# Optimization experiments

Measured on AMD Instinct MI355X. Metric: run time of the kernel, lower is better.

The kernel has to match this reference:

```python
import jax, jax.numpy as jnp
import numpy as np

N = 50000      # nodes
E = 400000     # edges (before self loops)
G = 8          # graphs in the batch
H = 128        # latent width (message_passer out_channels)
F_IN = 5       # raw node features
F_MASK = 3     # mask features (last col = BC indicator)
F_EDGE = 3     # edge_feature_dim
OUT = 3        # x-vel, y-vel, pressure
REPEATS = 3    # message passing rounds


def _mlp2(x, W1, b1, W2, b2):
    return jax.nn.relu(x @ W1 + b1) @ W2 + b2


def _seg_mean(v, ids, num):
    s = jax.ops.segment_sum(v, ids, num_segments=num)
    c = jax.ops.segment_sum(jnp.ones((v.shape[0],), v.dtype), ids, num_segments=num)
    return s / jnp.maximum(c, 1.0)[:, None]


def setup_inputs() -> dict:
    key = jax.random.key(0)
    ks = jax.random.split(key, 16)
    x = jax.random.normal(ks[0], (N, F_IN), jnp.float32)
    x_mask = (jax.random.uniform(ks[1], (N, F_MASK)) < 0.2).astype(jnp.float32)
    edge_index = jax.random.randint(ks[2], (2, E), 0, N, dtype=jnp.int32)
    edge_attr = jax.random.normal(ks[3], (E, F_EDGE), jnp.float32)
    pos = jax.random.uniform(ks[4], (N, 2), dtype=jnp.float32)
    batch = jnp.sort(jax.random.randint(ks[5], (N,), 0, G, dtype=jnp.int32))
    lin = lambda k, i, o: jax.random.normal(k, (i, o), jnp.float32) * (1.0 / np.sqrt(i))
    return {
        'x': x, 'x_mask': x_mask, 'edge_attr': edge_attr, 'pos': pos,
        'W_e1': lin(ks[6], F_IN + F_MASK, H), 'b_e1': jnp.zeros((H,), jnp.float32),
        'W_e2': lin(ks[7], H, H), 'b_e2': jnp.zeros((H,), jnp.float32),
        'W_m1': lin(ks[8], 2 * H + F_EDGE, H), 'b_m1': jnp.zeros((H,), jnp.float32),
        'W_m2': lin(ks[9], H, H), 'b_m2': jnp.zeros((H,), jnp.float32),
        'W_u1': lin(ks[10], 4 * H, H), 'b_u1': jnp.zeros((H,), jnp.float32),
        'W_u2': lin(ks[11], H, H), 'b_u2': jnp.zeros((H,), jnp.float32),
        'W_d1': lin(ks[12], H, H), 'b_d1': jnp.zeros((H,), jnp.float32),
        'W_d2': lin(ks[13], H, OUT), 'b_d2': jnp.zeros((OUT,), jnp.float32),
        'edge_index': edge_index, 'batch': batch,
    }


def reference(x, x_mask, edge_attr, pos,
              W_e1, b_e1, W_e2, b_e2,
              W_m1, b_m1, W_m2, b_m2,
              W_u1, b_u1, W_u2, b_u2,
              W_d1, b_d1, W_d2, b_d2,
              edge_index, batch):
    n = x.shape[0]
    bc = x_mask[:, -1]                                   # BC indicator (0/1)
    h = jnp.concatenate([x, x_mask], axis=1)             # [N, F_IN+F_MASK]
    # add self loops with zero edge attributes
    sl = jnp.arange(n, dtype=edge_index.dtype)
    ei = jnp.concatenate([edge_index, jnp.stack([sl, sl])], axis=1)
    ea = jnp.concatenate([edge_attr, jnp.zeros((n, edge_attr.shape[1]), edge_attr.dtype)], axis=0)
    # encoder
    h = _mlp2(h, W_e1, b_e1, W_e2, b_e2)                 # [N, H]
    # BC scatter-mean per graph and global mean pool
    bc_cnt = jax.ops.segment_sum(bc, batch, num_segments=G)
    x_BC = jax.ops.segment_sum(h * bc[:, None], batch, num_segments=G) / jnp.maximum(bc_cnt, 1.0)[:, None]
    x_graph = _seg_mean(h, batch, G)
    src, dst = ei[0], ei[1]
    for _ in range(REPEATS):
        m = _mlp2(jnp.concatenate([h[src], h[dst], ea], axis=1), W_m1, b_m1, W_m2, b_m2)
        agg = _seg_mean(m, dst, n)                       # mean aggregation at dst
        upd_in = jnp.concatenate([h, agg, x_graph[batch], x_BC[batch]], axis=1)
        h = h + _mlp2(upd_in, W_u1, b_u1, W_u2, b_u2)
        x_graph = _seg_mean(h, batch, G)
    return _mlp2(h, W_d1, b_d1, W_d2, b_d2)              # [N, OUT]
```

## Files before the change

### kernel.cpp

```cpp
#include <hip/hip_runtime.h>


#define NN 50000
#define EE 400000
#define GG 8
#define NBLK 196
#define SGRID 512

typedef __attribute__((ext_vector_type(8))) short short8;
typedef __attribute__((ext_vector_type(4))) float floatx4;

__device__ __forceinline__ unsigned short f2bf(float x) {
    unsigned u = __float_as_uint(x);
    u += 0x7FFF + ((u >> 16) & 1);
    return (unsigned short)(u >> 16);
}
__device__ __forceinline__ float bf2f(unsigned short h) {
    return __uint_as_float(((unsigned)h) << 16);
}
__device__ __forceinline__ void cvt8(const float* v, short8& hi, short8& lo) {
#pragma unroll
    for (int j = 0; j < 8; ++j) {
        unsigned short h = f2bf(v[j]);
        hi[j] = (short)h;
        lo[j] = (short)f2bf(v[j] - bf2f(h));
    }
}

__global__ void k_count(const int* __restrict__ ei, int* __restrict__ deg) {
    int i = blockIdx.x * 256 + threadIdx.x;
    if (i < EE) atomicAdd(&deg[ei[EE + i]], 1);
}

__global__ __launch_bounds__(256) void k_scan1(const int* __restrict__ deg, int* __restrict__ ex,
                                               int* __restrict__ blksum) {
    __shared__ int s[256];
    const int t = threadIdx.x;
    int i = blockIdx.x * 256 + t;
    int v = (i < NN) ? deg[i] : 0;
    s[t] = v;
    __syncthreads();
    for (int off = 1; off < 256; off <<= 1) {
        int x = (t >= off) ? s[t - off] : 0;
        __syncthreads();
        s[t] += x;
        __syncthreads();
    }
    if (i < NN) ex[i] = s[t] - v;
    if (t == 255) blksum[blockIdx.x] = s[255];
}

__global__ __launch_bounds__(256) void k_scan2(int* __restrict__ blksum) {
    __shared__ int s[256];
    const int t = threadIdx.x;
    int v = (t < NBLK) ? blksum[t] : 0;
    s[t] = v;
    __syncthreads();
    for (int off = 1; off < 256; off <<= 1) {
        int x = (t >= off) ? s[t - off] : 0;
        __syncthreads();
        s[t] += x;
        __syncthreads();
    }
    if (t < NBLK) blksum[t] = s[t] - v;
}

__global__ void k_scan3(const int* __restrict__ ex, const int* __restrict__ blkoff,
                        int* __restrict__ row_ptr, int* __restrict__ cursor) {
    int i = blockIdx.x * 256 + threadIdx.x;
    if (i < NN) {
        int v = ex[i] + blkoff[blockIdx.x];
        row_ptr[i] = v;
        cursor[i] = v;
    }
    if (i == 0) row_ptr[NN] = EE;
}

__global__ void k_scatter(const int* __restrict__ ei, const float* __restrict__ ea,
                          int* __restrict__ cursor, int* __restrict__ src_sorted,
                          float4* __restrict__ ea_s) {
    int e = blockIdx.x * 256 + threadIdx.x;
    if (e >= EE) return;
    int s = ei[e], d = ei[EE + e];
    int p = atomicAdd(&cursor[d], 1);
    src_sorted[p] = s;
    ea_s[p] = make_float4(ea[3 * e], ea[3 * e + 1], ea[3 * e + 2], 0.f);
}

__global__ __launch_bounds__(256) void k_counts(const int* __restrict__ batch, const float* __restrict__ xm,
                                                float* __restrict__ cnt_node, float* __restrict__ cnt_bc) {
    __shared__ float cn[8], cb[8];
    const int t = threadIdx.x;
    if (t < 8) { cn[t] = 0.f; cb[t] = 0.f; }
    __syncthreads();
    int i = blockIdx.x * 256 + t;
    if (i < NN) {
        int g = batch[i];
        atomicAdd(&cn[g], 1.f);
        atomicAdd(&cb[g], xm[3 * i + 2]);
    }
    __syncthreads();
    if (t < 8) {
        if (cn[t] != 0.f) atomicAdd(&cnt_node[t], cn[t]);
        if (cb[t] != 0.f) atomicAdd(&cnt_bc[t], cb[t]);
    }
}

__global__ __launch_bounds__(256) void k_wfuse(const float* __restrict__ Wm2, const float* __restrict__ Wu1,
                                               float* __restrict__ Wf) {
    int idx = blockIdx.x * 256 + threadIdx.x;
    int r = idx >> 7, c = idx & 127;
    float s = 0.f;
    for (int k = 0; k < 128; ++k) s += Wm2[r * 128 + k] * Wu1[(128 + k) * 128 + c];
    Wf[idx] = s;
}
__global__ void k_bfuse(const float* __restrict__ bm2, const float* __restrict__ Wu1,
                        const float* __restrict__ bu1, float* __restrict__ bf) {
    int c = threadIdx.x;
    float s = bu1[c];
    for (int k = 0; k < 128; ++k) s += bm2[k] * Wu1[(128 + k) * 128 + c];
    bf[c] = s;
}

__global__ __launch_bounds__(256) void k_pack_all(
    const float* __restrict__ We2, const float* __restrict__ Wm1,
    const float* __restrict__ Wu1, const float* __restrict__ Wf,
    const float* __restrict__ Wu2, const float* __restrict__ Wd1,
    short* __restrict__ We2h, short* __restrict__ We2l,
    short* __restrict__ Wm1sh, short* __restrict__ Wm1sl,
    short* __restrict__ Wm1dh, short* __restrict__ Wm1dl,
    short* __restrict__ Wu1ah, short* __restrict__ Wu1al,
    short* __restrict__ Wfh, short* __restrict__ Wfl,
    short* __restrict__ Wu2h, short* __restrict__ Wu2l,
    short* __restrict__ Wd1h, short* __restrict__ Wd1l) {
    int b = blockIdx.x;
    int id = b >> 6;
    int p = (b & 63) * 256 + threadIdx.x;
    const float* W;
    short *hi, *lo;
    switch (id) {
        case 0: W = We2; hi = We2h; lo = We2l; break;
        case 1: W = Wm1; hi = Wm1sh; lo = Wm1sl; break;
        case 2: W = Wm1 + 16384; hi = Wm1dh; lo = Wm1dl; break;
        case 3: W = Wu1; hi = Wu1ah; lo = Wu1al; break;
        case 4: W = Wf; hi = Wfh; lo = Wfl; break;
        case 5: W = Wu2; hi = Wu2h; lo = Wu2l; break;
        default: W = Wd1; hi = Wd1h; lo = Wd1l; break;
    }
    int j = p & 7;
    int lane = (p >> 3) & 63;
    int chunk = p >> 9;
    int k0 = chunk & 3, nt = chunk >> 2;
    int quad = lane >> 4;
    int n = nt * 16 + (lane & 15);
    int k;
    if (id == 5) k = k0 * 32 + ((j >> 2) << 4) + (quad << 2) + (j & 3);
    else k = k0 * 32 + quad * 8 + j;
    float w = W[k * 128 + n];
    unsigned short h = f2bf(w);
    hi[p] = (short)h;
    lo[p] = (short)f2bf(w - bf2f(h));
}

__global__ __launch_bounds__(256, 2) void k_genc(
    const float* __restrict__ x, const float* __restrict__ xm,
    const float* __restrict__ We1, const float* __restrict__ be1,
    const short* __restrict__ W2h, const short* __restrict__ W2l,
    const float* __restrict__ be2, const int* __restrict__ batch,
    float* __restrict__ hout, float* __restrict__ part_h, float* __restrict__ part_hbc) {
    __shared__ __align__(16) short sWh[16384];
    __shared__ __align__(16) short sWl[16384];
    __shared__ __align__(16) float swe[1024];
    __shared__ float sbe[128];
    __shared__ float ldsH[1024];
    __shared__ float ldsB[1024];
    const int tid = threadIdx.x;
    const int wave = tid >> 6, lane = tid & 63;
    const int m16 = lane & 15, quad = lane >> 4;
    const int t0 = blockIdx.x * 4 + wave;
    const int t1 = t0 + SGRID * 4;
    const bool h1 = (t1 < 3125);
    const int r0 = t0 * 16 + m16;
    const int r1 = (h1 ? t1 * 16 : 0) + m16;
    {
        const float4* sH = (const float4*)W2h;
        const float4* sL = (const float4*)W2l;
        float4* dH = (float4*)sWh;
        float4* dL = (float4*)sWl;
#pragma unroll
        for (int u = 0; u < 8; ++u) {
            int i = tid + u * 256;
            dH[i] = sH[i];
            dL[i] = sL[i];
        }
        for (int i = tid; i < 1024; i += 256) {
            swe[i] = We1[i];
            ldsH[i] = 0.f;
            ldsB[i] = 0.f;
        }
        if (tid < 128) sbe[tid] = be1[tid];
    }
    float in0[8], in1[8];
#pragma unroll
    for (int k = 0; k < 5; ++k) { in0[k] = x[r0 * 5 + k]; in1[k] = x[r1 * 5 + k]; }
#pragma unroll
    for (int k = 0; k < 3; ++k) { in0[5 + k] = xm[r0 * 3 + k]; in1[5 + k] = xm[r1 * 3 + k]; }
    int g0 = batch[r0], g1 = batch[r1];
    __syncthreads();
    short8 ah0[4], al0[4], ah1[4], al1[4];
#pragma unroll
    for (int k0 = 0; k0 < 4; ++k0) {
        float tv[8];
#pragma unroll
        for (int j = 0; j < 8; ++j) {
            int c = k0 * 32 + quad * 8 + j;
            float s = sbe[c];
#pragma unroll
            for (int kk = 0; kk < 8; ++kk) s += in0[kk] * swe[kk * 128 + c];
            tv[j] = fmaxf(s, 0.f);
        }
        cvt8(tv, ah0[k0], al0[k0]);
    }
#pragma unroll
    for (int k0 = 0; k0 < 4; ++k0) {
        float tv[8];
#pragma unroll
        for (int j = 0; j < 8; ++j) {
            int c = k0 * 32 + quad * 8 + j;
            float s = sbe[c];
#pragma unroll
            for (int kk = 0; kk < 8; ++kk) s += in1[kk] * swe[kk * 128 + c];
            tv[j] = fmaxf(s, 0.f);
        }
        cvt8(tv, ah1[k0], al1[k0]);
    }
    const int fb = lane << 3;
    floatx4 acc0[8], acc1[8];
#pragma unroll
    for (int nt = 0; nt < 8; ++nt) { acc0[nt] = (floatx4)0.f; acc1[nt] = (floatx4)0.f; }
#pragma unroll
    for (int k0 = 0; k0 < 4; ++k0) {
#pragma unroll
        for (int nt = 0; nt < 8; ++nt) {
            const int base = (((nt << 2) | k0) << 9) + fb;
            short8 bh = *(const short8*)&sWh[base];
            short8 bl = *(const short8*)&sWl[base];
            acc0[nt] = __builtin_amdgcn_mfma_f32_16x16x32_bf16(bh, ah0[k0], acc0[nt], 0, 0, 0);
            acc0[nt] = __builtin_amdgcn_mfma_f32_16x16x32_bf16(bl, ah0[k0], acc0[nt], 0, 0, 0);
            acc0[nt] = __builtin_amdgcn_mfma_f32_16x16x32_bf16(bh, al0[k0], acc0[nt], 0, 0, 0);
            if (h1) {
                acc1[nt] = __builtin_amdgcn_mfma_f32_16x16x32_bf16(bh, ah1[k0], acc1[nt], 0, 0, 0);
                acc1[nt] = __builtin_amdgcn_mfma_f32_16x16x32_bf16(bl, ah1[k0], acc1[nt], 0, 0, 0);
                acc1[nt] = __builtin_amdgcn_mfma_f32_16x16x32_bf16(bh, al1[k0], acc1[nt], 0, 0, 0);
            }
        }
    }
    float o0[8][4], o1[8][4];
#pragma unroll
    for (int nt = 0; nt < 8; ++nt) {
        float4 bv = *(const float4*)(be2 + nt * 16 + quad * 4);
#pragma unroll
        for (int i = 0; i < 4; ++i) {
            float b = (i == 0) ? bv.x : (i == 1) ? bv.y : (i == 2) ? bv.z : bv.w;
            o0[nt][i] = acc0[nt][i] + b;
            o1[nt][i] = acc1[nt][i] + b;
        }
    }
    {
        float* d0 = hout + (size_t)r0 * 128 + quad * 4;
#pragma unroll
        for (int nt = 0; nt < 8; ++nt)
            *(float4*)(d0 + nt * 16) = make_float4(o0[nt][0], o0[nt][1], o0[nt][2], o0[nt][3]);
    }
    if (h1) {
        float* d1 = hout + (size_t)r1 * 128 + quad * 4;
#pragma unroll
        for (int nt = 0; nt < 8; ++nt)
            *(float4*)(d1 + nt * 16) = make_float4(o1[nt][0], o1[nt][1], o1[nt][2], o1[nt][3]);
    }
    {
        float bc = in0[7];
        int glo = __shfl(g0, 0), ghi = __shfl(g0, 15);
        if (glo == ghi) {
#pragma unroll
            for (int nt = 0; nt < 8; ++nt) {
                float4 v = make_float4(o0[nt][0], o0[nt][1], o0[nt][2], o0[nt][3]);
                float4 w = make_float4(v.x * bc, v.y * bc, v.z * bc, v.w * bc);
#pragma unroll
                for (int off = 1; off < 16; off <<= 1) {
                    v.x += __shfl_xor(v.x, off); v.y += __shfl_xor(v.y, off);
                    v.z += __shfl_xor(v.z, off); v.w += __shfl_xor(v.w, off);
                    w.x += __shfl_xor(w.x, off); w.y += __shfl_xor(w.y, off);
                    w.z += __shfl_xor(w.z, off); w.w += __shfl_xor(w.w, off);
                }
                if (m16 == 0) {
                    float* sp = &ldsH[glo * 128 + nt * 16 + quad * 4];
                    atomicAdd(sp + 0, v.x); atomicAdd(sp + 1, v.y);
                    atomicAdd(sp + 2, v.z); atomicAdd(sp + 3, v.w);
                    float* sq = &ldsB[glo * 128 + nt * 16 + quad * 4];
                    atomicAdd(sq + 0, w.x); atomicAdd(sq + 1, w.y);
                    atomicAdd(sq + 2, w.z); atomicAdd(sq + 3, w.w);
                }
            }
        } else {
#pragma unroll
            for (int nt = 0; nt < 8; ++nt)
#pragma unroll
                for (int i = 0; i < 4; ++i) {
                    atomicAdd(&ldsH[g0 * 128 + nt * 16 + quad * 4 + i], o0[nt][i]);
                    atomicAdd(&ldsB[g0 * 128 + nt * 16 + quad * 4 + i], o0[nt][i] * bc);
                }
        }
    }
    if (h1) {
        float bc = in1[7];
        int glo = __shfl(g1, 0), ghi = __shfl(g1, 15);
        if (glo == ghi) {
#pragma unroll
            for (int nt = 0; nt < 8; ++nt) {
                float4 v = make_float4(o1[nt][0], o1[nt][1], o1[nt][2], o1[nt][3]);
                float4 w = make_float4(v.x * bc, v.y * bc, v.z * bc, v.w * bc);
#pragma unroll
                for (int off = 1; off < 16; off <<= 1) {
                    v.x += __shfl_xor(v.x, off); v.y += __shfl_xor(v.y, off);
                    v.z += __shfl_xor(v.z, off); v.w += __shfl_xor(v.w, off);
                    w.x += __shfl_xor(w.x, off); w.y += __shfl_xor(w.y, off);
                    w.z += __shfl_xor(w.z, off); w.w += __shfl_xor(w.w, off);
                }
                if (m16 == 0) {
                    float* sp = &ldsH[glo * 128 + nt * 16 + quad * 4];
                    atomicAdd(sp + 0, v.x); atomicAdd(sp + 1, v.y);
                    atomicAdd(sp + 2, v.z); atomicAdd(sp + 3, v.w);
                    float* sq = &ldsB[glo * 128 + nt * 16 + quad * 4];
                    atomicAdd(sq + 0, w.x); atomicAdd(sq + 1, w.y);
                    atomicAdd(sq + 2, w.z); atomicAdd(sq + 3, w.w);
                }
            }
        } else {
#pragma unroll
            for (int nt = 0; nt < 8; ++nt)
#pragma unroll
                for (int i = 0; i < 4; ++i) {
                    atomicAdd(&ldsH[g1 * 128 + nt * 16 + quad * 4 + i], o1[nt][i]);
                    atomicAdd(&ldsB[g1 * 128 + nt * 16 + quad * 4 + i], o1[nt][i] * bc);
                }
        }
    }
    __syncthreads();
    {
        float* ph = part_h + (size_t)blockIdx.x * 1024;
        float* pb = part_hbc + (size_t)blockIdx.x * 1024;
        for (int i = tid; i < 1024; i += 256) { ph[i] = ldsH[i]; pb[i] = ldsB[i]; }
    }
}

__global__ __launch_bounds__(128) void k_redstats(const float* __restrict__ part_h,
                                                  const float* __restrict__ part_hbc,
                                                  float* __restrict__ sum_h, float* __restrict__ sum_hbc) {
    const int g = blockIdx.x, c = threadIdx.x;
    float s = 0.f, sb = 0.f;
    for (int b = 0; b < SGRID; ++b) {
        s += part_h[b * 1024 + g * 128 + c];
        sb += part_hbc[b * 1024 + g * 128 + c];
    }
    sum_h[g * 128 + c] = s;
    sum_hbc[g * 128 + c] = sb;
}

__global__ __launch_bounds__(256, 2) void k_gemm2(
    const float* __restrict__ A,
    const short* __restrict__ W1h, const short* __restrict__ W1l,
    const short* __restrict__ W2h, const short* __restrict__ W2l,
    const float* __restrict__ bias2,
    float* __restrict__ out1, float* __restrict__ out2) {
    __shared__ __align__(16) short sWh[16384];
    __shared__ __align__(16) short sWl[16384];
    const int tid = threadIdx.x;
    const int wave = tid >> 6, lane = tid & 63;
    const int m16 = lane & 15, quad = lane >> 4;
    const int t0 = blockIdx.x * 4 + wave;
    const int t1 = t0 + SGRID * 4;
    const bool h1 = (t1 < 3125);
    const int r0 = t0 * 16 + m16;
    const int r1 = (h1 ? t1 * 16 : 0) + m16;

    auto copyW = [&](const short* gh, const short* gl) {
        const float4* sH = (const float4*)gh;
        const float4* sL = (const float4*)gl;
        float4* dH = (float4*)sWh;
        float4* dL = (float4*)sWl;
#pragma unroll
        for (int u = 0; u < 8; ++u) {
            int i = tid + u * 256;
            dH[i] = sH[i];
            dL[i] = sL[i];
        }
    };

    const float* Ap0 = A + (size_t)r0 * 128 + quad * 8;
    const float* Ap1 = A + (size_t)r1 * 128 + quad * 8;
    float4 a0[8], a1[8];
#pragma unroll
    for (int k0 = 0; k0 < 4; ++k0) {
        a0[k0 * 2 + 0] = *(const float4*)(Ap0 + k0 * 32);
        a0[k0 * 2 + 1] = *(const float4*)(Ap0 + k0 * 32 + 4);
        a1[k0 * 2 + 0] = *(const float4*)(Ap1 + k0 * 32);
        a1[k0 * 2 + 1] = *(const float4*)(Ap1 + k0 * 32 + 4);
    }
    copyW(W1h, W1l);
    __syncthreads();

    short8 ah0[4], al0[4], ah1[4], al1[4];
#pragma unroll
    for (int k0 = 0; k0 < 4; ++k0) {
        float v[8] = {a0[k0 * 2].x, a0[k0 * 2].y, a0[k0 * 2].z, a0[k0 * 2].w,
                      a0[k0 * 2 + 1].x, a0[k0 * 2 + 1].y, a0[k0 * 2 + 1].z, a0[k0 * 2 + 1].w};
        cvt8(v, ah0[k0], al0[k0]);
    }
#pragma unroll
    for (int k0 = 0; k0 < 4; ++k0) {
        float v[8] = {a1[k0 * 2].x, a1[k0 * 2].y, a1[k0 * 2].z, a1[k0 * 2].w,
                      a1[k0 * 2 + 1].x, a1[k0 * 2 + 1].y, a1[k0 * 2 + 1].z, a1[k0 * 2 + 1].w};
        cvt8(v, ah1[k0], al1[k0]);
    }

    const int fb = lane << 3;
    floatx4 acc0[8], acc1[8];
    auto mmacc = [&]() {
#pragma unroll
        for (int nt = 0; nt < 8; ++nt) {
            acc0[nt] = (floatx4)0.f;
            acc1[nt] = (floatx4)0.f;
        }
#pragma unroll
        for (int k0 = 0; k0 < 4; ++k0) {
#pragma unroll
            for (int nt = 0; nt < 8; ++nt) {
                const int base = (((nt << 2) | k0) << 9) + fb;
                short8 bh = *(const short8*)&sWh[base];
                short8 bl = *(const short8*)&sWl[base];
                acc0[nt] = __builtin_amdgcn_mfma_f32_16x16x32_bf16(bh, ah0[k0], acc0[nt], 0, 0, 0);
                acc0[nt] = __builtin_amdgcn_mfma_f32_16x16x32_bf16(bl, ah0[k0], acc0[nt], 0, 0, 0);
                acc0[nt] = __builtin_amdgcn_mfma_f32_16x16x32_bf16(bh, al0[k0], acc0[nt], 0, 0, 0);
                if (h1) {
                    acc1[nt] = __builtin_amdgcn_mfma_f32_16x16x32_bf16(bh, ah1[k0], acc1[nt], 0, 0, 0);
                    acc1[nt] = __builtin_amdgcn_mfma_f32_16x16x32_bf16(bl, ah1[k0], acc1[nt], 0, 0, 0);
                    acc1[nt] = __builtin_amdgcn_mfma_f32_16x16x32_bf16(bh, al1[k0], acc1[nt], 0, 0, 0);
                }
            }
        }
    };

    mmacc();
    {
        float* d0 = out1 + (size_t)r0 * 128 + quad * 4;
        float* d1 = out1 + (size_t)r1 * 128 + quad * 4;
#pragma unroll
        for (int nt = 0; nt < 8; ++nt)
            *(float4*)(d0 + nt * 16) = make_float4(acc0[nt][0], acc0[nt][1], acc0[nt][2], acc0[nt][3]);
        if (h1) {
#pragma unroll
            for (int nt = 0; nt < 8; ++nt)
                *(float4*)(d1 + nt * 16) = make_float4(acc1[nt][0], acc1[nt][1], acc1[nt][2], acc1[nt][3]);
        }
    }
    __syncthreads();
    copyW(W2h, W2l);
    __syncthreads();
    mmacc();
    {
        float* d0 = out2 + (size_t)r0 * 128 + quad * 4;
        float* d1 = out2 + (size_t)r1 * 128 + quad * 4;
#pragma unroll
        for (int nt = 0; nt < 8; ++nt) {
            float4 bv = *(const float4*)(bias2 + nt * 16 + quad * 4);
            *(float4*)(d0 + nt * 16) = make_float4(acc0[nt][0] + bv.x, acc0[nt][1] + bv.y,
                                                   acc0[nt][2] + bv.z, acc0[nt][3] + bv.w);
            if (h1)
                *(float4*)(d1 + nt * 16) = make_float4(acc1[nt][0] + bv.x, acc1[nt][1] + bv.y,
                                                       acc1[nt][2] + bv.z, acc1[nt][3] + bv.w);
        }
    }
}

template <bool STATS>
__global__ __launch_bounds__(256, 2) void k_fused3(
    const float* __restrict__ hbuf, const float* __restrict__ accm,
    const short* __restrict__ W1h, const short* __restrict__ W1l,
    const short* __restrict__ W2h, const short* __restrict__ W2l,
    const short* __restrict__ W3h, const short* __restrict__ W3l,
    const float* __restrict__ gt, const float* __restrict__ bf3,
    const float* __restrict__ bu2, const int* __restrict__ batch,
    float* __restrict__ hout, float* __restrict__ partf) {
    __shared__ __align__(16) short sWh[16384];
    __shared__ __align__(16) short sWl[16384];
    __shared__ float ldsH[1024];
    const int tid = threadIdx.x;
    const int wave = tid >> 6, lane = tid & 63;
    const int m16 = lane & 15, quad = lane >> 4;
    const int t0 = blockIdx.x * 4 + wave;
    const int t1 = t0 + SGRID * 4;
    const bool h1 = (t1 < 3125);
    const int r0 = t0 * 16 + m16;
    const int r1 = (h1 ? t1 * 16 : 0) + m16;

    auto copyW = [&](const short* gh, const short* gl) {
        const float4* sH = (const float4*)gh;
        const float4* sL = (const float4*)gl;
        float4* dH = (float4*)sWh;
        float4* dL = (float4*)sWl;
#pragma unroll
        for (int u = 0; u < 8; ++u) {
            int i = tid + u * 256;
            dH[i] = sH[i];
            dL[i] = sL[i];
        }
    };

    const float* Ap0 = hbuf + (size_t)r0 * 128 + quad * 8;
    const float* Ap1 = hbuf + (size_t)r1 * 128 + quad * 8;
    float4 a0[8], a1[8];
#pragma unroll
    for (int k0 = 0; k0 < 4; ++k0) {
        a0[k0 * 2 + 0] = *(const float4*)(Ap0 + k0 * 32);
        a0[k0 * 2 + 1] = *(const float4*)(Ap0 + k0 * 32 + 4);
        a1[k0 * 2 + 0] = *(const float4*)(Ap1 + k0 * 32);
        a1[k0 * 2 + 1] = *(const float4*)(Ap1 + k0 * 32 + 4);
    }
    int g0 = batch[r0], g1 = batch[r1];
    if (STATS) {
        for (int i = tid; i < 1024; i += 256) ldsH[i] = 0.f;
    }
    copyW(W1h, W1l);
    __syncthreads();

    short8 hh0[4], hl0[4], hh1[4], hl1[4];
#pragma unroll
    for (int k0 = 0; k0 < 4; ++k0) {
        float v[8] = {a0[k0 * 2].x, a0[k0 * 2].y, a0[k0 * 2].z, a0[k0 * 2].w,
                      a0[k0 * 2 + 1].x, a0[k0 * 2 + 1].y, a0[k0 * 2 + 1].z, a0[k0 * 2 + 1].w};
        cvt8(v, hh0[k0], hl0[k0]);
    }
#pragma unroll
    for (int k0 = 0; k0 < 4; ++k0) {
        float v[8] = {a1[k0 * 2].x, a1[k0 * 2].y, a1[k0 * 2].z, a1[k0 * 2].w,
                      a1[k0 * 2 + 1].x, a1[k0 * 2 + 1].y, a1[k0 * 2 + 1].z, a1[k0 * 2 + 1].w};
        cvt8(v, hh1[k0], hl1[k0]);
    }

    const int fb = lane << 3;
    floatx4 acc0[8], acc1[8];
    auto mmacc = [&](const short8 xh0[4], const short8 xl0[4],
                     const short8 xh1[4], const short8 xl1[4]) {
#pragma unroll
        for (int k0 = 0; k0 < 4; ++k0) {
#pragma unroll
            for (int nt = 0; nt < 8; ++nt) {
                const int base = (((nt << 2) | k0) << 9) + fb;
                short8 bh = *(const short8*)&sWh[base];
                short8 bl = *(const short8*)&sWl[base];
                acc0[nt] = __builtin_amdgcn_mfma_f32_16x16x32_bf16(bh, xh0[k0], acc0[nt], 0, 0, 0);
                acc0[nt] = __builtin_amdgcn_mfma_f32_16x16x32_bf16(bl, xh0[k0], acc0[nt], 0, 0, 0);
                acc0[nt] = __builtin_amdgcn_mfma_f32_16x16x32_bf16(bh, xl0[k0], acc0[nt], 0, 0, 0);
                if (h1) {
                    acc1[nt] = __builtin_amdgcn_mfma_f32_16x16x32_bf16(bh, xh1[k0], acc1[nt], 0, 0, 0);
                    acc1[nt] = __builtin_amdgcn_mfma_f32_16x16x32_bf16(bl, xh1[k0], acc1[nt], 0, 0, 0);
                    acc1[nt] = __builtin_amdgcn_mfma_f32_16x16x32_bf16(bh, xl1[k0], acc1[nt], 0, 0, 0);
                }
            }
        }
    };

    {
        const float* gp0 = gt + g0 * 128 + quad * 4;
        const float* gp1 = gt + g1 * 128 + quad * 4;
#pragma unroll
        for (int nt = 0; nt < 8; ++nt) {
            float4 bv = *(const float4*)(bf3 + nt * 16 + quad * 4);
            float4 gv0 = *(const float4*)(gp0 + nt * 16);
            float4 gv1 = *(const float4*)(gp1 + nt * 16);
            acc0[nt][0] = bv.x + gv0.x; acc0[nt][1] = bv.y + gv0.y;
            acc0[nt][2] = bv.z + gv0.z; acc0[nt][3] = bv.w + gv0.w;
            acc1[nt][0] = bv.x + gv1.x; acc1[nt][1] = bv.y + gv1.y;
            acc1[nt][2] = bv.z + gv1.z; acc1[nt][3] = bv.w + gv1.w;
        }
    }
    mmacc(hh0, hl0, hh1, hl1);

    const float* Cp0 = accm + (size_t)r0 * 128 + quad * 8;
    const float* Cp1 = accm + (size_t)r1 * 128 + quad * 8;
    float4 c0[8], c1[8];
#pragma unroll
    for (int k0 = 0; k0 < 4; ++k0) {
        c0[k0 * 2 + 0] = *(const float4*)(Cp0 + k0 * 32);
        c0[k0 * 2 + 1] = *(const float4*)(Cp0 + k0 * 32 + 4);
        c1[k0 * 2 + 0] = *(const float4*)(Cp1 + k0 * 32);
        c1[k0 * 2 + 1] = *(const float4*)(Cp1 + k0 * 32 + 4);
    }
    __syncthreads();
    copyW(W2h, W2l);
    __syncthreads();

    short8 ch0[4], cl0[4], ch1[4], cl1[4];
#pragma unroll
    for (int k0 = 0; k0 < 4; ++k0) {
        float v[8] = {c0[k0 * 2].x, c0[k0 * 2].y, c0[k0 * 2].z, c0[k0 * 2].w,
                      c0[k0 * 2 + 1].x, c0[k0 * 2 + 1].y, c0[k0 * 2 + 1].z, c0[k0 * 2 + 1].w};
        cvt8(v, ch0[k0], cl0[k0]);
    }
#pragma unroll
    for (int k0 = 0; k0 < 4; ++k0) {
        float v[8] = {c1[k0 * 2].x, c1[k0 * 2].y, c1[k0 * 2].z, c1[k0 * 2].w,
                      c1[k0 * 2 + 1].x, c1[k0 * 2 + 1].y, c1[k0 * 2 + 1].z, c1[k0 * 2 + 1].w};
        cvt8(v, ch1[k0], cl1[k0]);
    }
    mmacc(ch0, cl0, ch1, cl1);

    short8 ph0[4], pl0[4], ph1[4], pl1[4];
#pragma unroll
    for (int k0 = 0; k0 < 4; ++k0) {
        float v[8] = {fmaxf(acc0[2 * k0][0], 0.f), fmaxf(acc0[2 * k0][1], 0.f),
                      fmaxf(acc0[2 * k0][2], 0.f), fmaxf(acc0[2 * k0][3], 0.f),
                      fmaxf(acc0[2 * k0 + 1][0], 0.f), fmaxf(acc0[2 * k0 + 1][1], 0.f),
                      fmaxf(acc0[2 * k0 + 1][2], 0.f), fmaxf(acc0[2 * k0 + 1][3], 0.f)};
        cvt8(v, ph0[k0], pl0[k0]);
    }
#pragma unroll
    for (int k0 = 0; k0 < 4; ++k0) {
        float v[8] = {fmaxf(acc1[2 * k0][0], 0.f), fmaxf(acc1[2 * k0][1], 0.f),
                      fmaxf(acc1[2 * k0][2], 0.f), fmaxf(acc1[2 * k0][3], 0.f),
                      fmaxf(acc1[2 * k0 + 1][0], 0.f), fmaxf(acc1[2 * k0 + 1][1], 0.f),
                      fmaxf(acc1[2 * k0 + 1][2], 0.f), fmaxf(acc1[2 * k0 + 1][3], 0.f)};
        cvt8(v, ph1[k0], pl1[k0]);
    }

    {
        const float* Ep0 = hbuf + (size_t)r0 * 128 + quad * 4;
        const float* Ep1 = hbuf + (size_t)r1 * 128 + quad * 4;
#pragma unroll
        for (int nt = 0; nt < 8; ++nt) {
            float4 bv = *(const float4*)(bu2 + nt * 16 + quad * 4);
            float4 e0 = *(const float4*)(Ep0 + nt * 16);
            float4 e1 = *(const float4*)(Ep1 + nt * 16);
            acc0[nt][0] = e0.x + bv.x; acc0[nt][1] = e0.y + bv.y;
            acc0[nt][2] = e0.z + bv.z; acc0[nt][3] = e0.w + bv.w;
            acc1[nt][0] = e1.x + bv.x; acc1[nt][1] = e1.y + bv.y;
            acc1[nt][2] = e1.z + bv.z; acc1[nt][3] = e1.w + bv.w;
        }
    }
    __syncthreads();
    copyW(W3h, W3l);
    __syncthreads();
    mmacc(ph0, pl0, ph1, pl1);

    {
        float* d0 = hout + (size_t)r0 * 128 + quad * 4;
#pragma unroll
        for (int nt = 0; nt < 8; ++nt)
            *(float4*)(d0 + nt * 16) = make_float4(acc0[nt][0], acc0[nt][1], acc0[nt][2], acc0[nt][3]);
    }
    if (h1) {
        float* d1 = hout + (size_t)r1 * 128 + quad * 4;
#pragma unroll
        for (int nt = 0; nt < 8; ++nt)
            *(float4*)(d1 + nt * 16) = make_float4(acc1[nt][0], acc1[nt][1], acc1[nt][2], acc1[nt][3]);
    }
    if (STATS) {
        {
            int glo = __shfl(g0, 0), ghi = __shfl(g0, 15);
            if (glo == ghi) {
#pragma unroll
                for (int nt = 0; nt < 8; ++nt) {
                    float4 v = make_float4(acc0[nt][0], acc0[nt][1], acc0[nt][2], acc0[nt][3]);
#pragma unroll
                    for (int off = 1; off < 16; off <<= 1) {
                        v.x += __shfl_xor(v.x, off);
                        v.y += __shfl_xor(v.y, off);
                        v.z += __shfl_xor(v.z, off);
                        v.w += __shfl_xor(v.w, off);
                    }
                    if (m16 == 0) {
                        float* sp = &ldsH[glo * 128 + nt * 16 + quad * 4];
                        atomicAdd(sp + 0, v.x); atomicAdd(sp + 1, v.y);
                        atomicAdd(sp + 2, v.z); atomicAdd(sp + 3, v.w);
                    }
                }
            } else {
#pragma unroll
                for (int nt = 0; nt < 8; ++nt)
#pragma unroll
                    for (int i = 0; i < 4; ++i)
                        atomicAdd(&ldsH[g0 * 128 + nt * 16 + quad * 4 + i], acc0[nt][i]);
            }
        }
        if (h1) {
            int glo = __shfl(g1, 0), ghi = __shfl(g1, 15);
            if (glo == ghi) {
#pragma unroll
                for (int nt = 0; nt < 8; ++nt) {
                    float4 v = make_float4(acc1[nt][0], acc1[nt][1], acc1[nt][2], acc1[nt][3]);
#pragma unroll
                    for (int off = 1; off < 16; off <<= 1) {
                        v.x += __shfl_xor(v.x, off);
                        v.y += __shfl_xor(v.y, off);
                        v.z += __shfl_xor(v.z, off);
                        v.w += __shfl_xor(v.w, off);
                    }
                    if (m16 == 0) {
                        float* sp = &ldsH[glo * 128 + nt * 16 + quad * 4];
                        atomicAdd(sp + 0, v.x); atomicAdd(sp + 1, v.y);
                        atomicAdd(sp + 2, v.z); atomicAdd(sp + 3, v.w);
                    }
                }
            } else {
#pragma unroll
                for (int nt = 0; nt < 8; ++nt)
#pragma unroll
                    for (int i = 0; i < 4; ++i)
                        atomicAdd(&ldsH[g1 * 128 + nt * 16 + quad * 4 + i], acc1[nt][i]);
            }
        }
        __syncthreads();
        float* pf = partf + (size_t)blockIdx.x * 1024;
        for (int i = tid; i < 1024; i += 256) pf[i] = ldsH[i];
    }
}

__global__ __launch_bounds__(256, 2) void k_gdec(
    const float* __restrict__ A, const short* __restrict__ W1h, const short* __restrict__ W1l,
    const float* __restrict__ bd1, const float* __restrict__ Wd2, const float* __restrict__ bd2,
    float* __restrict__ out) {
    __shared__ __align__(16) short sWh[16384];
    __shared__ __align__(16) short sWl[16384];
    const int tid = threadIdx.x;
    const int wave = tid >> 6, lane = tid & 63;
    const int m16 = lane & 15, quad = lane >> 4;
    const int t0 = blockIdx.x * 4 + wave;
    const int t1 = t0 + SGRID * 4;
    const bool h1 = (t1 < 3125);
    const int r0 = t0 * 16 + m16;
    const int r1 = (h1 ? t1 * 16 : 0) + m16;
    {
        const float4* sH = (const float4*)W1h;
        const float4* sL = (const float4*)W1l;
        float4* dH = (float4*)sWh;
        float4* dL = (float4*)sWl;
#pragma unroll
        for (int u = 0; u < 8; ++u) {
            int i = tid + u * 256;
            dH[i] = sH[i];
            dL[i] = sL[i];
        }
    }
    const float* Ap0 = A + (size_t)r0 * 128 + quad * 8;
    const float* Ap1 = A + (size_t)r1 * 128 + quad * 8;
    float4 a0[8], a1[8];
#pragma unroll
    for (int k0 = 0; k0 < 4; ++k0) {
        a0[k0 * 2 + 0] = *(const float4*)(Ap0 + k0 * 32);
        a0[k0 * 2 + 1] = *(const float4*)(Ap0 + k0 * 32 + 4);
        a1[k0 * 2 + 0] = *(const float4*)(Ap1 + k0 * 32);
        a1[k0 * 2 + 1] = *(const float4*)(Ap1 + k0 * 32 + 4);
    }
    __syncthreads();
    short8 ah0[4], al0[4], ah1[4], al1[4];
#pragma unroll
    for (int k0 = 0; k0 < 4; ++k0) {
        float v[8] = {a0[k0 * 2].x, a0[k0 * 2].y, a0[k0 * 2].z, a0[k0 * 2].w,
                      a0[k0 * 2 + 1].x, a0[k0 * 2 + 1].y, a0[k0 * 2 + 1].z, a0[k0 * 2 + 1].w};
        cvt8(v, ah0[k0], al0[k0]);
    }
#pragma unroll
    for (int k0 = 0; k0 < 4; ++k0) {
        float v[8] = {a1[k0 * 2].x, a1[k0 * 2].y, a1[k0 * 2].z, a1[k0 * 2].w,
                      a1[k0 * 2 + 1].x, a1[k0 * 2 + 1].y, a1[k0 * 2 + 1].z, a1[k0 * 2 + 1].w};
        cvt8(v, ah1[k0], al1[k0]);
    }
    const int fb = lane << 3;
    floatx4 acc0[8], acc1[8];
#pragma unroll
    for (int nt = 0; nt < 8; ++nt) { acc0[nt] = (floatx4)0.f; acc1[nt] = (floatx4)0.f; }
#pragma unroll
    for (int k0 = 0; k0 < 4; ++k0) {
#pragma unroll
        for (int nt = 0; nt < 8; ++nt) {
            const int base = (((nt << 2) | k0) << 9) + fb;
            short8 bh = *(const short8*)&sWh[base];
            short8 bl = *(const short8*)&sWl[base];
            acc0[nt] = __builtin_amdgcn_mfma_f32_16x16x32_bf16(bh, ah0[k0], acc0[nt], 0, 0, 0);
            acc0[nt] = __builtin_amdgcn_mfma_f32_16x16x32_bf16(bl, ah0[k0], acc0[nt], 0, 0, 0);
            acc0[nt] = __builtin_amdgcn_mfma_f32_16x16x32_bf16(bh, al0[k0], acc0[nt], 0, 0, 0);
            if (h1) {
                acc1[nt] = __builtin_amdgcn_mfma_f32_16x16x32_bf16(bh, ah1[k0], acc1[nt], 0, 0, 0);
                acc1[nt] = __builtin_amdgcn_mfma_f32_16x16x32_bf16(bl, ah1[k0], acc1[nt], 0, 0, 0);
                acc1[nt] = __builtin_amdgcn_mfma_f32_16x16x32_bf16(bh, al1[k0], acc1[nt], 0, 0, 0);
            }
        }
    }
    float p00 = 0.f, p01 = 0.f, p02 = 0.f, p10 = 0.f, p11 = 0.f, p12 = 0.f;
#pragma unroll
    for (int nt = 0; nt < 8; ++nt) {
        float4 bv = *(const float4*)(bd1 + nt * 16 + quad * 4);
#pragma unroll
        for (int i = 0; i < 4; ++i) {
            float b = (i == 0) ? bv.x : (i == 1) ? bv.y : (i == 2) ? bv.z : bv.w;
            int c = nt * 16 + quad * 4 + i;
            const float* wp = &Wd2[c * 3];
            float v0 = fmaxf(acc0[nt][i] + b, 0.f);
            float v1 = fmaxf(acc1[nt][i] + b, 0.f);
            p00 += v0 * wp[0]; p01 += v0 * wp[1]; p02 += v0 * wp[2];
            p10 += v1 * wp[0]; p11 += v1 * wp[1]; p12 += v1 * wp[2];
        }
    }
    p00 += __shfl_xor(p00, 16); p00 += __shfl_xor(p00, 32);
    p01 += __shfl_xor(p01, 16); p01 += __shfl_xor(p01, 32);
    p02 += __shfl_xor(p02, 16); p02 += __shfl_xor(p02, 32);
    p10 += __shfl_xor(p10, 16); p10 += __shfl_xor(p10, 32);
    p11 += __shfl_xor(p11, 16); p11 += __shfl_xor(p11, 32);
    p12 += __shfl_xor(p12, 16); p12 += __shfl_xor(p12, 32);
    if (quad == 0) {
        out[r0 * 3 + 0] = p00 + bd2[0];
        out[r0 * 3 + 1] = p01 + bd2[1];
        out[r0 * 3 + 2] = p02 + bd2[2];
        if (h1) {
            out[r1 * 3 + 0] = p10 + bd2[0];
            out[r1 * 3 + 1] = p11 + bd2[1];
            out[r1 * 3 + 2] = p12 + bd2[2];
        }
    }
}

__global__ __launch_bounds__(256) void k_edge_agg(const float* __restrict__ Ps, const float* __restrict__ Pd,
                                                  const int* __restrict__ row_ptr, const int* __restrict__ src_sorted,
                                                  const float4* __restrict__ ea_s, const float* __restrict__ Wm1,
                                                  float* __restrict__ accm) {
    const int lane = threadIdx.x & 63;
    const int d = blockIdx.x * 4 + (threadIdx.x >> 6);
    const int c = lane * 2;
    const float2 w0 = *(const float2*)&Wm1[256 * 128 + c];
    const float2 w1 = *(const float2*)&Wm1[257 * 128 + c];
    const float2 w2 = *(const float2*)&Wm1[258 * 128 + c];
    const float2 pd = *(const float2*)&Pd[(size_t)d * 128 + c];
    const int beg = row_ptr[d], end = row_ptr[d + 1];
    const float2 sv = *(const float2*)&Ps[(size_t)d * 128 + c];
    float ax = fmaxf(sv.x + pd.x, 0.f);
    float ay = fmaxf(sv.y + pd.y, 0.f);
    int k = beg;
    for (; k + 3 < end; k += 4) {
        int s0 = src_sorted[k], s1 = src_sorted[k + 1], s2 = src_sorted[k + 2], s3 = src_sorted[k + 3];
        float4 e0 = ea_s[k], e1 = ea_s[k + 1], e2 = ea_s[k + 2], e3 = ea_s[k + 3];
        float2 pa = *(const float2*)&Ps[(size_t)s0 * 128 + c];
        float2 pb = *(const float2*)&Ps[(size_t)s1 * 128 + c];
        float2 pc = *(const float2*)&Ps[(size_t)s2 * 128 + c];
        float2 pe = *(const float2*)&Ps[(size_t)s3 * 128 + c];
        ax += fmaxf(pa.x + pd.x + e0.x * w0.x + e0.y * w1.x + e0.z * w2.x, 0.f)
            + fmaxf(pb.x + pd.x + e1.x * w0.x + e1.y * w1.x + e1.z * w2.x, 0.f)
            + fmaxf(pc.x + pd.x + e2.x * w0.x + e2.y * w1.x + e2.z * w2.x, 0.f)
            + fmaxf(pe.x + pd.x + e3.x * w0.x + e3.y * w1.x + e3.z * w2.x, 0.f);
        ay += fmaxf(pa.y + pd.y + e0.x * w0.y + e0.y * w1.y + e0.z * w2.y, 0.f)
            + fmaxf(pb.y + pd.y + e1.x * w0.y + e1.y * w1.y + e1.z * w2.y, 0.f)
            + fmaxf(pc.y + pd.y + e2.x * w0.y + e2.y * w1.y + e2.z * w2.y, 0.f)
            + fmaxf(pe.y + pd.y + e3.x * w0.y + e3.y * w1.y + e3.z * w2.y, 0.f);
    }
    for (; k < end; ++k) {
        int s0 = src_sorted[k];
        float4 e0 = ea_s[k];
        float2 pa = *(const float2*)&Ps[(size_t)s0 * 128 + c];
        ax += fmaxf(pa.x + pd.x + e0.x * w0.x + e0.y * w1.x + e0.z * w2.x, 0.f);
        ay += fmaxf(pa.y + pd.y + e0.x * w0.y + e0.y * w1.y + e0.z * w2.y, 0.f);
    }
    float inv = 1.f / (float)(end - beg + 1);
    *(float2*)&accm[(size_t)d * 128 + c] = make_float2(ax * inv, ay * inv);
}

template <bool PART>
__global__ __launch_bounds__(128) void k_gterm(const float* __restrict__ sum_h, const float* __restrict__ sum_hbc,
                                               const float* __restrict__ partf,
                                               const float* __restrict__ cnt_node, const float* __restrict__ cnt_bc,
                                               const float* __restrict__ Wu1, float* __restrict__ gt) {
    const int g = blockIdx.x;
    const int c = threadIdx.x;
    __shared__ float sg[128], sb[128];
    const float invn = 1.f / fmaxf(cnt_node[g], 1.f);
    const float invb = 1.f / fmaxf(cnt_bc[g], 1.f);
    float s0;
    if (PART) {
        s0 = 0.f;
        for (int b = 0; b < SGRID; ++b) s0 += partf[b * 1024 + g * 128 + c];
    } else {
        s0 = sum_h[g * 128 + c];
    }
    sg[c] = s0 * invn;
    sb[c] = sum_hbc[g * 128 + c] * invb;
    __syncthreads();
    float s = 0.f;
    for (int k = 0; k < 128; ++k) s += sg[k] * Wu1[(256 + k) * 128 + c];
    for (int k = 0; k < 128; ++k) s += sb[k] * Wu1[(384 + k) * 128 + c];
    gt[g * 128 + c] = s;
}

extern "C" void kernel_launch(void* const* d_in, const int* in_sizes, int n_in,
                              void* d_out, int out_size, void* d_ws, size_t ws_size,
                              hipStream_t stream) {
    const float* x = (const float*)d_in[0];
    const float* x_mask = (const float*)d_in[1];
    const float* edge_attr = (const float*)d_in[2];
    const float* W_e1 = (const float*)d_in[4];
    const float* b_e1 = (const float*)d_in[5];
    const float* W_e2 = (const float*)d_in[6];
    const float* b_e2 = (const float*)d_in[7];
    const float* W_m1 = (const float*)d_in[8];
    const float* b_m1 = (const float*)d_in[9];
    const float* W_m2 = (const float*)d_in[10];
    const float* b_m2 = (const float*)d_in[11];
    const float* W_u1 = (const float*)d_in[12];
    const float* b_u1 = (const float*)d_in[13];
    const float* W_u2 = (const float*)d_in[14];
    const float* b_u2 = (const float*)d_in[15];
    const float* W_d1 = (const float*)d_in[16];
    const float* b_d1 = (const float*)d_in[17];
    const float* W_d2 = (const float*)d_in[18];
    const float* b_d2 = (const float*)d_in[19];
    const int* edge_index = (const int*)d_in[20];
    const int* batch = (const int*)d_in[21];
    float* out = (float*)d_out;

    char* wp = (char*)d_ws;
    auto carve = [&](size_t bytes) {
        char* r = wp;
        wp += (bytes + 255) & ~(size_t)255;
        return r;
    };
    float* h = (float*)carve(sizeof(float) * (size_t)NN * 128);
    float* Ps = (float*)carve(sizeof(float) * (size_t)NN * 128);
    float* Pd = (float*)carve(sizeof(float) * (size_t)NN * 128);
    float* accm = (float*)carve(sizeof(float) * (size_t)NN * 128);
    float4* ea_s = (float4*)carve(sizeof(float4) * (size_t)EE);
    float* stats = (float*)carve(sizeof(float) * 4096);
    float* sum_h = stats;
    float* sum_hbc = stats + 1024;
    float* cnt_node = stats + 2048;
    float* cnt_bc = stats + 2056;
    float* gterm = stats + 2304;
    float* bfused = stats + 3328;
    float* part_h = (float*)carve(sizeof(float) * (size_t)SGRID * 1024);
    float* part_hbc = (float*)carve(sizeof(float) * (size_t)SGRID * 1024);
    float* partf = (float*)carve(sizeof(float) * (size_t)SGRID * 1024);
    int* deg = (int*)carve(sizeof(int) * NN);
    int* row_ptr = (int*)carve(sizeof(int) * (NN + 1));
    int* cursor = (int*)carve(sizeof(int) * NN);
    int* src_sorted = (int*)carve(sizeof(int) * EE);
    int* exbuf = (int*)carve(sizeof(int) * NN);
    int* blksum = (int*)carve(sizeof(int) * 256);
    float* Wf = (float*)carve(sizeof(float) * 16384);
    short* We2h = (short*)carve(sizeof(short) * 16384);
    short* We2l = (short*)carve(sizeof(short) * 16384);
    short* Wm1sh = (short*)carve(sizeof(short) * 16384);
    short* Wm1sl = (short*)carve(sizeof(short) * 16384);
    short* Wm1dh = (short*)carve(sizeof(short) * 16384);
    short* Wm1dl = (short*)carve(sizeof(short) * 16384);
    short* Wu1ah = (short*)carve(sizeof(short) * 16384);
    short* Wu1al = (short*)carve(sizeof(short) * 16384);
    short* Wfh = (short*)carve(sizeof(short) * 16384);
    short* Wfl = (short*)carve(sizeof(short) * 16384);
    short* Wu2h = (short*)carve(sizeof(short) * 16384);
    short* Wu2l = (short*)carve(sizeof(short) * 16384);
    short* Wd1h = (short*)carve(sizeof(short) * 16384);
    short* Wd1l = (short*)carve(sizeof(short) * 16384);

    const dim3 b256(256);
    const int gE256 = (EE + 255) / 256;

    hipMemsetAsync(deg, 0, sizeof(int) * NN, stream);
    hipMemsetAsync(stats, 0, sizeof(float) * 2064, stream);
    k_wfuse<<<64, b256, 0, stream>>>(W_m2, W_u1, Wf);
    k_bfuse<<<1, 128, 0, stream>>>(b_m2, W_u1, b_u1, bfused);
    k_pack_all<<<448, b256, 0, stream>>>(W_e2, W_m1, W_u1, Wf, W_u2, W_d1,
                                         We2h, We2l, Wm1sh, Wm1sl, Wm1dh, Wm1dl,
                                         Wu1ah, Wu1al, Wfh, Wfl, Wu2h, Wu2l, Wd1h, Wd1l);
    k_count<<<gE256, b256, 0, stream>>>(edge_index, deg);
    k_scan1<<<NBLK, b256, 0, stream>>>(deg, exbuf, blksum);
    k_scan2<<<1, b256, 0, stream>>>(blksum);
    k_scan3<<<NBLK, b256, 0, stream>>>(exbuf, blksum, row_ptr, cursor);
    k_scatter<<<gE256, b256, 0, stream>>>(edge_index, edge_attr, cursor, src_sorted, ea_s);
    k_counts<<<NBLK, b256, 0, stream>>>(batch, x_mask, cnt_node, cnt_bc);
    k_genc<<<SGRID, b256, 0, stream>>>(x, x_mask, W_e1, b_e1, We2h, We2l, b_e2,
                                       batch, h, part_h, part_hbc);
    k_redstats<<<GG, 128, 0, stream>>>(part_h, part_hbc, sum_h, sum_hbc);

    for (int rep = 0; rep < 3; ++rep) {
        if (rep == 0)
            k_gterm<false><<<GG, 128, 0, stream>>>(sum_h, sum_hbc, nullptr, cnt_node, cnt_bc, W_u1, gterm);
        else
            k_gterm<true><<<GG, 128, 0, stream>>>(nullptr, sum_hbc, partf, cnt_node, cnt_bc, W_u1, gterm);
        k_gemm2<<<SGRID, b256, 0, stream>>>(h, Wm1sh, Wm1sl, Wm1dh, Wm1dl, b_m1, Ps, Pd);
        k_edge_agg<<<NN / 4, b256, 0, stream>>>(Ps, Pd, row_ptr, src_sorted, ea_s, W_m1, accm);
        if (rep < 2) {
            k_fused3<true><<<SGRID, b256, 0, stream>>>(h, accm, Wu1ah, Wu1al, Wfh, Wfl,
                                                       Wu2h, Wu2l, gterm, bfused, b_u2,
                                                       batch, h, partf);
        } else {
            k_fused3<false><<<SGRID, b256, 0, stream>>>(h, accm, Wu1ah, Wu1al, Wfh, Wfl,
                                                        Wu2h, Wu2l, gterm, bfused, b_u2,
                                                        batch, h, nullptr);
        }
    }
    k_gdec<<<SGRID, b256, 0, stream>>>(h, Wd1h, Wd1l, b_d1, W_d2, b_d2, out);
}
```

Baseline: 639.6 us.

## Fuse Ps/Pd projection GEMMs into encoder and update kernels, fold decoder into last update

Removes the standalone k_gemm2 and k_gdec kernels. The src/dst projections of the message MLP are now computed directly from register-held h in the encoder and in each update kernel, and the decoder runs inside the final update kernel. Weight packing for Wm1 and Wd1 is permuted so that MFMA accumulator output can feed the next MFMA as its input without a shuffle. This saves re-reading h from global memory and several kernel launches, at the cost of longer kernels with more register pressure and extra LDS weight reloads.

```diff
diff --git a/kernel.cpp b/kernel.cpp
--- a/kernel.cpp
+++ b/kernel.cpp
@@ -153,8 +153,9 @@
     int k0 = chunk & 3, nt = chunk >> 2;
     int quad = lane >> 4;
     int n = nt * 16 + (lane & 15);
+    bool perm = (id == 1) || (id == 2) || (id == 5) || (id == 6);
     int k;
-    if (id == 5) k = k0 * 32 + ((j >> 2) << 4) + (quad << 2) + (j & 3);
+    if (perm) k = k0 * 32 + ((j >> 2) << 4) + (quad << 2) + (j & 3);
     else k = k0 * 32 + quad * 8 + j;
     float w = W[k * 128 + n];
     unsigned short h = f2bf(w);
@@ -166,8 +167,12 @@
     const float* __restrict__ x, const float* __restrict__ xm,
     const float* __restrict__ We1, const float* __restrict__ be1,
     const short* __restrict__ W2h, const short* __restrict__ W2l,
-    const float* __restrict__ be2, const int* __restrict__ batch,
-    float* __restrict__ hout, float* __restrict__ part_h, float* __restrict__ part_hbc) {
+    const float* __restrict__ be2,
+    const short* __restrict__ Wsh, const short* __restrict__ Wsl,
+    const short* __restrict__ Wdh, const short* __restrict__ Wdl,
+    const float* __restrict__ bm1, const int* __restrict__ batch,
+    float* __restrict__ hout, float* __restrict__ Ps, float* __restrict__ Pd,
+    float* __restrict__ part_h, float* __restrict__ part_hbc) {
     __shared__ __align__(16) short sWh[16384];
     __shared__ __align__(16) short sWl[16384];
     __shared__ __align__(16) float swe[1024];
@@ -182,9 +187,10 @@
     const bool h1 = (t1 < 3125);
     const int r0 = t0 * 16 + m16;
     const int r1 = (h1 ? t1 * 16 : 0) + m16;
-    {
-        const float4* sH = (const float4*)W2h;
-        const float4* sL = (const float4*)W2l;
+
+    auto copyW = [&](const short* gh, const short* gl) {
+        const float4* sH = (const float4*)gh;
+        const float4* sL = (const float4*)gl;
         float4* dH = (float4*)sWh;
         float4* dL = (float4*)sWl;
 #pragma unroll
@@ -193,6 +199,10 @@
             dH[i] = sH[i];
             dL[i] = sL[i];
         }
+    };
+
+    {
+        copyW(W2h, W2l);
         for (int i = tid; i < 1024; i += 256) {
             swe[i] = We1[i];
             ldsH[i] = 0.f;
@@ -236,47 +246,45 @@
     }
     const int fb = lane << 3;
     floatx4 acc0[8], acc1[8];
-#pragma unroll
-    for (int nt = 0; nt < 8; ++nt) { acc0[nt] = (floatx4)0.f; acc1[nt] = (floatx4)0.f; }
-#pragma unroll
-    for (int k0 = 0; k0 < 4; ++k0) {
-#pragma unroll
-        for (int nt = 0; nt < 8; ++nt) {
-            const int base = (((nt << 2) | k0) << 9) + fb;
-            short8 bh = *(const short8*)&sWh[base];
-            short8 bl = *(const short8*)&sWl[base];
-            acc0[nt] = __builtin_amdgcn_mfma_f32_16x16x32_bf16(bh, ah0[k0], acc0[nt], 0, 0, 0);
-            acc0[nt] = __builtin_amdgcn_mfma_f32_16x16x32_bf16(bl, ah0[k0], acc0[nt], 0, 0, 0);
-            acc0[nt] = __builtin_amdgcn_mfma_f32_16x16x32_bf16(bh, al0[k0], acc0[nt], 0, 0, 0);
-            if (h1) {
-                acc1[nt] = __builtin_amdgcn_mfma_f32_16x16x32_bf16(bh, ah1[k0], acc1[nt], 0, 0, 0);
-                acc1[nt] = __builtin_amdgcn_mfma_f32_16x16x32_bf16(bl, ah1[k0], acc1[nt], 0, 0, 0);
-                acc1[nt] = __builtin_amdgcn_mfma_f32_16x16x32_bf16(bh, al1[k0], acc1[nt], 0, 0, 0);
+    auto mmacc = [&](const short8 xh0[4], const short8 xl0[4],
+                     const short8 xh1[4], const short8 xl1[4]) {
+#pragma unroll
+        for (int k0 = 0; k0 < 4; ++k0) {
+#pragma unroll
+            for (int nt = 0; nt < 8; ++nt) {
+                const int base = (((nt << 2) | k0) << 9) + fb;
+                short8 bh = *(const short8*)&sWh[base];
+                short8 bl = *(const short8*)&sWl[base];
+                acc0[nt] = __builtin_amdgcn_mfma_f32_16x16x32_bf16(bh, xh0[k0], acc0[nt], 0, 0, 0);
+                acc0[nt] = __builtin_amdgcn_mfma_f32_16x16x32_bf16(bl, xh0[k0], acc0[nt], 0, 0, 0);
+                acc0[nt] = __builtin_amdgcn_mfma_f32_16x16x32_bf16(bh, xl0[k0], acc0[nt], 0, 0, 0);
+                if (h1) {
+                    acc1[nt] = __builtin_amdgcn_mfma_f32_16x16x32_bf16(bh, xh1[k0], acc1[nt], 0, 0, 0);
+                    acc1[nt] = __builtin_amdgcn_mfma_f32_16x16x32_bf16(bl, xh1[k0], acc1[nt], 0, 0, 0);
+                    acc1[nt] = __builtin_amdgcn_mfma_f32_16x16x32_bf16(bh, xl1[k0], acc1[nt], 0, 0, 0);
+                }
             }
         }
-    }
-    float o0[8][4], o1[8][4];
+    };
+
 #pragma unroll
     for (int nt = 0; nt < 8; ++nt) {
         float4 bv = *(const float4*)(be2 + nt * 16 + quad * 4);
-#pragma unroll
-        for (int i = 0; i < 4; ++i) {
-            float b = (i == 0) ? bv.x : (i == 1) ? bv.y : (i == 2) ? bv.z : bv.w;
-            o0[nt][i] = acc0[nt][i] + b;
-            o1[nt][i] = acc1[nt][i] + b;
-        }
-    }
+        acc0[nt][0] = bv.x; acc0[nt][1] = bv.y; acc0[nt][2] = bv.z; acc0[nt][3] = bv.w;
+        acc1[nt][0] = bv.x; acc1[nt][1] = bv.y; acc1[nt][2] = bv.z; acc1[nt][3] = bv.w;
+    }
+    mmacc(ah0, al0, ah1, al1);
     {
         float* d0 = hout + (size_t)r0 * 128 + quad * 4;
 #pragma unroll
         for (int nt = 0; nt < 8; ++nt)
-            *(float4*)(d0 + nt * 16) = make_float4(o0[nt][0], o0[nt][1], o0[nt][2], o0[nt][3]);
+            *(float4*)(d0 + nt * 16) = make_float4(acc0[nt][0], acc0[nt][1], acc0[nt][2], acc0[nt][3]);
     }
     if (h1) {
         float* d1 = hout + (size_t)r1 * 128 + quad * 4;
 #pragma unroll
         for (int nt = 0; nt < 8; ++nt)
-            *(float4*)(d1 + nt * 16) = make_float4(o1[nt][0], o1[nt][1], o1[nt][2], o1[nt][3]);
+            *(float4*)(d1 + nt * 16) = make_float4(acc1[nt][0], acc1[nt][1], acc1[nt][2], acc1[nt][3]);
     }
     {
         float bc = in0[7];
@@ -284,7 +292,7 @@
         if (glo == ghi) {
 #pragma unroll
             for (int nt = 0; nt < 8; ++nt) {
-                float4 v = make_float4(o0[nt][0], o0[nt][1], o0[nt][2], o0[nt][3]);
+                float4 v = make_float4(acc0[nt][0], acc0[nt][1], acc0[nt][2], acc0[nt][3]);
                 float4 w = make_float4(v.x * bc, v.y * bc, v.z * bc, v.w * bc);
 #pragma unroll
                 for (int off = 1; off < 16; off <<= 1) {
@@ -307,8 +315,8 @@
             for (int nt = 0; nt < 8; ++nt)
 #pragma unroll
                 for (int i = 0; i < 4; ++i) {
-                    atomicAdd(&ldsH[g0 * 128 + nt * 16 + quad * 4 + i], o0[nt][i]);
-                    atomicAdd(&ldsB[g0 * 128 + nt * 16 + quad * 4 + i], o0[nt][i] * bc);
+                    atomicAdd(&ldsH[g0 * 128 + nt * 16 + quad * 4 + i], acc0[nt][i]);
+                    atomicAdd(&ldsB[g0 * 128 + nt * 16 + quad * 4 + i], acc0[nt][i] * bc);
                 }
         }
     }
@@ -318,7 +326,7 @@
         if (glo == ghi) {
 #pragma unroll
             for (int nt = 0; nt < 8; ++nt) {
-                float4 v = make_float4(o1[nt][0], o1[nt][1], o1[nt][2], o1[nt][3]);
+                float4 v = make_float4(acc1[nt][0], acc1[nt][1], acc1[nt][2], acc1[nt][3]);
                 float4 w = make_float4(v.x * bc, v.y * bc, v.z * bc, v.w * bc);
 #pragma unroll
                 for (int off = 1; off < 16; off <<= 1) {
@@ -341,16 +349,68 @@
             for (int nt = 0; nt < 8; ++nt)
 #pragma unroll
                 for (int i = 0; i < 4; ++i) {
-                    atomicAdd(&ldsH[g1 * 128 + nt * 16 + quad * 4 + i], o1[nt][i]);
-                    atomicAdd(&ldsB[g1 * 128 + nt * 16 + quad * 4 + i], o1[nt][i] * bc);
+                    atomicAdd(&ldsH[g1 * 128 + nt * 16 + quad * 4 + i], acc1[nt][i]);
+                    atomicAdd(&ldsB[g1 * 128 + nt * 16 + quad * 4 + i], acc1[nt][i] * bc);
                 }
         }
+    }
+    short8 ph0[4], pl0[4], ph1[4], pl1[4];
+#pragma unroll
+    for (int k0 = 0; k0 < 4; ++k0) {
+        float v[8] = {acc0[2 * k0][0], acc0[2 * k0][1], acc0[2 * k0][2], acc0[2 * k0][3],
+                      acc0[2 * k0 + 1][0], acc0[2 * k0 + 1][1], acc0[2 * k0 + 1][2], acc0[2 * k0 + 1][3]};
+        cvt8(v, ph0[k0], pl0[k0]);
+    }
+#pragma unroll
+    for (int k0 = 0; k0 < 4; ++k0) {
+        float v[8] = {acc1[2 * k0][0], acc1[2 * k0][1], acc1[2 * k0][2], acc1[2 * k0][3],
+                      acc1[2 * k0 + 1][0], acc1[2 * k0 + 1][1], acc1[2 * k0 + 1][2], acc1[2 * k0 + 1][3]};
+        cvt8(v, ph1[k0], pl1[k0]);
     }
     __syncthreads();
     {
         float* ph = part_h + (size_t)blockIdx.x * 1024;
         float* pb = part_hbc + (size_t)blockIdx.x * 1024;
         for (int i = tid; i < 1024; i += 256) { ph[i] = ldsH[i]; pb[i] = ldsB[i]; }
+    }
+    copyW(Wsh, Wsl);
+    __syncthreads();
+#pragma unroll
+    for (int nt = 0; nt < 8; ++nt) { acc0[nt] = (floatx4)0.f; acc1[nt] = (floatx4)0.f; }
+    mmacc(ph0, pl0, ph1, pl1);
+    {
+        float* d0 = Ps + (size_t)r0 * 128 + quad * 4;
+#pragma unroll
+        for (int nt = 0; nt < 8; ++nt)
+            *(float4*)(d0 + nt * 16) = make_float4(acc0[nt][0], acc0[nt][1], acc0[nt][2], acc0[nt][3]);
+        if (h1) {
+            float* d1 = Ps + (size_t)r1 * 128 + quad * 4;
+#pragma unroll
+            for (int nt = 0; nt < 8; ++nt)
+                *(float4*)(d1 + nt * 16) = make_float4(acc1[nt][0], acc1[nt][1], acc1[nt][2], acc1[nt][3]);
+        }
+    }
+    __syncthreads();
+    copyW(Wdh, Wdl);
+    __syncthreads();
+#pragma unroll
+    for (int nt = 0; nt < 8; ++nt) {
+        float4 bv = *(const float4*)(bm1 + nt * 16 + quad * 4);
+        acc0[nt][0] = bv.x; acc0[nt][1] = bv.y; acc0[nt][2] = bv.z; acc0[nt][3] = bv.w;
+        acc1[nt][0] = bv.x; acc1[nt][1] = bv.y; acc1[nt][2] = bv.z; acc1[nt][3] = bv.w;
+    }
+    mmacc(ph0, pl0, ph1, pl1);
+    {
+        float* d0 = Pd + (size_t)r0 * 128 + quad * 4;
+#pragma unroll
+        for (int nt = 0; nt < 8; ++nt)
+            *(float4*)(d0 + nt * 16) = make_float4(acc0[nt][0], acc0[nt][1], acc0[nt][2], acc0[nt][3]);
+        if (h1) {
+            float* d1 = Pd + (size_t)r1 * 128 + quad * 4;
+#pragma unroll
+            for (int nt = 0; nt < 8; ++nt)
+                *(float4*)(d1 + nt * 16) = make_float4(acc1[nt][0], acc1[nt][1], acc1[nt][2], acc1[nt][3]);
+        }
     }
 }
 
@@ -367,131 +427,20 @@
     sum_hbc[g * 128 + c] = sb;
 }
 
-__global__ __launch_bounds__(256, 2) void k_gemm2(
-    const float* __restrict__ A,
-    const short* __restrict__ W1h, const short* __restrict__ W1l,
-    const short* __restrict__ W2h, const short* __restrict__ W2l,
-    const float* __restrict__ bias2,
-    float* __restrict__ out1, float* __restrict__ out2) {
-    __shared__ __align__(16) short sWh[16384];
-    __shared__ __align__(16) short sWl[16384];
-    const int tid = threadIdx.x;
-    const int wave = tid >> 6, lane = tid & 63;
-    const int m16 = lane & 15, quad = lane >> 4;
-    const int t0 = blockIdx.x * 4 + wave;
-    const int t1 = t0 + SGRID * 4;
-    const bool h1 = (t1 < 3125);
-    const int r0 = t0 * 16 + m16;
-    const int r1 = (h1 ? t1 * 16 : 0) + m16;
-
-    auto copyW = [&](const short* gh, const short* gl) {
-        const float4* sH = (const float4*)gh;
-        const float4* sL = (const float4*)gl;
-        float4* dH = (float4*)sWh;
-        float4* dL = (float4*)sWl;
-#pragma unroll
-        for (int u = 0; u < 8; ++u) {
-            int i = tid + u * 256;
-            dH[i] = sH[i];
-            dL[i] = sL[i];
-        }
-    };
-
-    const float* Ap0 = A + (size_t)r0 * 128 + quad * 8;
-    const float* Ap1 = A + (size_t)r1 * 128 + quad * 8;
-    float4 a0[8], a1[8];
-#pragma unroll
-    for (int k0 = 0; k0 < 4; ++k0) {
-        a0[k0 * 2 + 0] = *(const float4*)(Ap0 + k0 * 32);
-        a0[k0 * 2 + 1] = *(const float4*)(Ap0 + k0 * 32 + 4);
-        a1[k0 * 2 + 0] = *(const float4*)(Ap1 + k0 * 32);
-        a1[k0 * 2 + 1] = *(const float4*)(Ap1 + k0 * 32 + 4);
-    }
-    copyW(W1h, W1l);
-    __syncthreads();
-
-    short8 ah0[4], al0[4], ah1[4], al1[4];
-#pragma unroll
-    for (int k0 = 0; k0 < 4; ++k0) {
-        float v[8] = {a0[k0 * 2].x, a0[k0 * 2].y, a0[k0 * 2].z, a0[k0 * 2].w,
-                      a0[k0 * 2 + 1].x, a0[k0 * 2 + 1].y, a0[k0 * 2 + 1].z, a0[k0 * 2 + 1].w};
-        cvt8(v, ah0[k0], al0[k0]);
-    }
-#pragma unroll
-    for (int k0 = 0; k0 < 4; ++k0) {
-        float v[8] = {a1[k0 * 2].x, a1[k0 * 2].y, a1[k0 * 2].z, a1[k0 * 2].w,
-                      a1[k0 * 2 + 1].x, a1[k0 * 2 + 1].y, a1[k0 * 2 + 1].z, a1[k0 * 2 + 1].w};
-        cvt8(v, ah1[k0], al1[k0]);
-    }
-
-    const int fb = lane << 3;
-    floatx4 acc0[8], acc1[8];
-    auto mmacc = [&]() {
-#pragma unroll
-        for (int nt = 0; nt < 8; ++nt) {
-            acc0[nt] = (floatx4)0.f;
-            acc1[nt] = (floatx4)0.f;
-        }
-#pragma unroll
-        for (int k0 = 0; k0 < 4; ++k0) {
-#pragma unroll
-            for (int nt = 0; nt < 8; ++nt) {
-                const int base = (((nt << 2) | k0) << 9) + fb;
-                short8 bh = *(const short8*)&sWh[base];
-                short8 bl = *(const short8*)&sWl[base];
-                acc0[nt] = __builtin_amdgcn_mfma_f32_16x16x32_bf16(bh, ah0[k0], acc0[nt], 0, 0, 0);
-                acc0[nt] = __builtin_amdgcn_mfma_f32_16x16x32_bf16(bl, ah0[k0], acc0[nt], 0, 0, 0);
-                acc0[nt] = __builtin_amdgcn_mfma_f32_16x16x32_bf16(bh, al0[k0], acc0[nt], 0, 0, 0);
-                if (h1) {
-                    acc1[nt] = __builtin_amdgcn_mfma_f32_16x16x32_bf16(bh, ah1[k0], acc1[nt], 0, 0, 0);
-                    acc1[nt] = __builtin_amdgcn_mfma_f32_16x16x32_bf16(bl, ah1[k0], acc1[nt], 0, 0, 0);
-                    acc1[nt] = __builtin_amdgcn_mfma_f32_16x16x32_bf16(bh, al1[k0], acc1[nt], 0, 0, 0);
-                }
-            }
-        }
-    };
-
-    mmacc();
-    {
-        float* d0 = out1 + (size_t)r0 * 128 + quad * 4;
-        float* d1 = out1 + (size_t)r1 * 128 + quad * 4;
-#pragma unroll
-        for (int nt = 0; nt < 8; ++nt)
-            *(float4*)(d0 + nt * 16) = make_float4(acc0[nt][0], acc0[nt][1], acc0[nt][2], acc0[nt][3]);
-        if (h1) {
-#pragma unroll
-            for (int nt = 0; nt < 8; ++nt)
-                *(float4*)(d1 + nt * 16) = make_float4(acc1[nt][0], acc1[nt][1], acc1[nt][2], acc1[nt][3]);
-        }
-    }
-    __syncthreads();
-    copyW(W2h, W2l);
-    __syncthreads();
-    mmacc();
-    {
-        float* d0 = out2 + (size_t)r0 * 128 + quad * 4;
-        float* d1 = out2 + (size_t)r1 * 128 + quad * 4;
-#pragma unroll
-        for (int nt = 0; nt < 8; ++nt) {
-            float4 bv = *(const float4*)(bias2 + nt * 16 + quad * 4);
-            *(float4*)(d0 + nt * 16) = make_float4(acc0[nt][0] + bv.x, acc0[nt][1] + bv.y,
-                                                   acc0[nt][2] + bv.z, acc0[nt][3] + bv.w);
-            if (h1)
-                *(float4*)(d1 + nt * 16) = make_float4(acc1[nt][0] + bv.x, acc1[nt][1] + bv.y,
-                                                       acc1[nt][2] + bv.z, acc1[nt][3] + bv.w);
-        }
-    }
-}
-
-template <bool STATS>
+template <int MODE>
 __global__ __launch_bounds__(256, 2) void k_fused3(
     const float* __restrict__ hbuf, const float* __restrict__ accm,
     const short* __restrict__ W1h, const short* __restrict__ W1l,
     const short* __restrict__ W2h, const short* __restrict__ W2l,
     const short* __restrict__ W3h, const short* __restrict__ W3l,
+    const short* __restrict__ Wsh, const short* __restrict__ Wsl,
+    const short* __restrict__ Wdh, const short* __restrict__ Wdl,
     const float* __restrict__ gt, const float* __restrict__ bf3,
-    const float* __restrict__ bu2, const int* __restrict__ batch,
-    float* __restrict__ hout, float* __restrict__ partf) {
+    const float* __restrict__ bu2, const float* __restrict__ bm1,
+    const float* __restrict__ bd1, const float* __restrict__ Wd2,
+    const float* __restrict__ bd2, const int* __restrict__ batch,
+    float* __restrict__ hout, float* __restrict__ Ps, float* __restrict__ Pd,
+    float* __restrict__ partf, float* __restrict__ outp) {
     __shared__ __align__(16) short sWh[16384];
     __shared__ __align__(16) short sWl[16384];
     __shared__ float ldsH[1024];
@@ -528,7 +477,7 @@
         a1[k0 * 2 + 1] = *(const float4*)(Ap1 + k0 * 32 + 4);
     }
     int g0 = batch[r0], g1 = batch[r1];
-    if (STATS) {
+    if (MODE == 0) {
         for (int i = tid; i < 1024; i += 256) ldsH[i] = 0.f;
     }
     copyW(W1h, W1l);
@@ -653,19 +602,19 @@
     __syncthreads();
     mmacc(ph0, pl0, ph1, pl1);
 
-    {
-        float* d0 = hout + (size_t)r0 * 128 + quad * 4;
-#pragma unroll
-        for (int nt = 0; nt < 8; ++nt)
-            *(float4*)(d0 + nt * 16) = make_float4(acc0[nt][0], acc0[nt][1], acc0[nt][2], acc0[nt][3]);
-    }
-    if (h1) {
-        float* d1 = hout + (size_t)r1 * 128 + quad * 4;
-#pragma unroll
-        for (int nt = 0; nt < 8; ++nt)
-            *(float4*)(d1 + nt * 16) = make_float4(acc1[nt][0], acc1[nt][1], acc1[nt][2], acc1[nt][3]);
-    }
-    if (STATS) {
+    if (MODE == 0) {
+        {
+            float* d0 = hout + (size_t)r0 * 128 + quad * 4;
+#pragma unroll
+            for (int nt = 0; nt < 8; ++nt)
+                *(float4*)(d0 + nt * 16) = make_float4(acc0[nt][0], acc0[nt][1], acc0[nt][2], acc0[nt][3]);
+        }
+        if (h1) {
+            float* d1 = hout + (size_t)r1 * 128 + quad * 4;
+#pragma unroll
+            for (int nt = 0; nt < 8; ++nt)
+                *(float4*)(d1 + nt * 16) = make_float4(acc1[nt][0], acc1[nt][1], acc1[nt][2], acc1[nt][3]);
+        }
         {
             int glo = __shfl(g0, 0), ghi = __shfl(g0, 15);
             if (glo == ghi) {
@@ -720,112 +669,113 @@
                         atomicAdd(&ldsH[g1 * 128 + nt * 16 + quad * 4 + i], acc1[nt][i]);
             }
         }
+#pragma unroll
+        for (int k0 = 0; k0 < 4; ++k0) {
+            float v[8] = {acc0[2 * k0][0], acc0[2 * k0][1], acc0[2 * k0][2], acc0[2 * k0][3],
+                          acc0[2 * k0 + 1][0], acc0[2 * k0 + 1][1], acc0[2 * k0 + 1][2], acc0[2 * k0 + 1][3]};
+            cvt8(v, ph0[k0], pl0[k0]);
+        }
+#pragma unroll
+        for (int k0 = 0; k0 < 4; ++k0) {
+            float v[8] = {acc1[2 * k0][0], acc1[2 * k0][1], acc1[2 * k0][2], acc1[2 * k0][3],
+                          acc1[2 * k0 + 1][0], acc1[2 * k0 + 1][1], acc1[2 * k0 + 1][2], acc1[2 * k0 + 1][3]};
+            cvt8(v, ph1[k0], pl1[k0]);
+        }
         __syncthreads();
-        float* pf = partf + (size_t)blockIdx.x * 1024;
-        for (int i = tid; i < 1024; i += 256) pf[i] = ldsH[i];
-    }
-}
-
-__global__ __launch_bounds__(256, 2) void k_gdec(
-    const float* __restrict__ A, const short* __restrict__ W1h, const short* __restrict__ W1l,
-    const float* __restrict__ bd1, const float* __restrict__ Wd2, const float* __restrict__ bd2,
-    float* __restrict__ out) {
-    __shared__ __align__(16) short sWh[16384];
-    __shared__ __align__(16) short sWl[16384];
-    const int tid = threadIdx.x;
-    const int wave = tid >> 6, lane = tid & 63;
-    const int m16 = lane & 15, quad = lane >> 4;
-    const int t0 = blockIdx.x * 4 + wave;
-    const int t1 = t0 + SGRID * 4;
-    const bool h1 = (t1 < 3125);
-    const int r0 = t0 * 16 + m16;
-    const int r1 = (h1 ? t1 * 16 : 0) + m16;
-    {
-        const float4* sH = (const float4*)W1h;
-        const float4* sL = (const float4*)W1l;
-        float4* dH = (float4*)sWh;
-        float4* dL = (float4*)sWl;
-#pragma unroll
-        for (int u = 0; u < 8; ++u) {
-            int i = tid + u * 256;
-            dH[i] = sH[i];
-            dL[i] = sL[i];
-        }
-    }
-    const float* Ap0 = A + (size_t)r0 * 128 + quad * 8;
-    const float* Ap1 = A + (size_t)r1 * 128 + quad * 8;
-    float4 a0[8], a1[8];
-#pragma unroll
-    for (int k0 = 0; k0 < 4; ++k0) {
-        a0[k0 * 2 + 0] = *(const float4*)(Ap0 + k0 * 32);
-        a0[k0 * 2 + 1] = *(const float4*)(Ap0 + k0 * 32 + 4);
-        a1[k0 * 2 + 0] = *(const float4*)(Ap1 + k0 * 32);
-        a1[k0 * 2 + 1] = *(const float4*)(Ap1 + k0 * 32 + 4);
-    }
-    __syncthreads();
-    short8 ah0[4], al0[4], ah1[4], al1[4];
-#pragma unroll
-    for (int k0 = 0; k0 < 4; ++k0) {
-        float v[8] = {a0[k0 * 2].x, a0[k0 * 2].y, a0[k0 * 2].z, a0[k0 * 2].w,
-                      a0[k0 * 2 + 1].x, a0[k0 * 2 + 1].y, a0[k0 * 2 + 1].z, a0[k0 * 2 + 1].w};
-        cvt8(v, ah0[k0], al0[k0]);
-    }
-#pragma unroll
-    for (int k0 = 0; k0 < 4; ++k0) {
-        float v[8] = {a1[k0 * 2].x, a1[k0 * 2].y, a1[k0 * 2].z, a1[k0 * 2].w,
-                      a1[k0 * 2 + 1].x, a1[k0 * 2 + 1].y, a1[k0 * 2 + 1].z, a1[k0 * 2 + 1].w};
-        cvt8(v, ah1[k0], al1[k0]);
-    }
-    const int fb = lane << 3;
-    floatx4 acc0[8], acc1[8];
-#pragma unroll
-    for (int nt = 0; nt < 8; ++nt) { acc0[nt] = (floatx4)0.f; acc1[nt] = (floatx4)0.f; }
-#pragma unroll
-    for (int k0 = 0; k0 < 4; ++k0) {
+        {
+            float* pf = partf + (size_t)blockIdx.x * 1024;
+            for (int i = tid; i < 1024; i += 256) pf[i] = ldsH[i];
+        }
+        copyW(Wsh, Wsl);
+        __syncthreads();
+#pragma unroll
+        for (int nt = 0; nt < 8; ++nt) { acc0[nt] = (floatx4)0.f; acc1[nt] = (floatx4)0.f; }
+        mmacc(ph0, pl0, ph1, pl1);
+        {
+            float* d0 = Ps + (size_t)r0 * 128 + quad * 4;
+#pragma unroll
+            for (int nt = 0; nt < 8; ++nt)
+                *(float4*)(d0 + nt * 16) = make_float4(acc0[nt][0], acc0[nt][1], acc0[nt][2], acc0[nt][3]);
+            if (h1) {
+                float* d1 = Ps + (size_t)r1 * 128 + quad * 4;
+#pragma unroll
+                for (int nt = 0; nt < 8; ++nt)
+                    *(float4*)(d1 + nt * 16) = make_float4(acc1[nt][0], acc1[nt][1], acc1[nt][2], acc1[nt][3]);
+            }
+        }
+        __syncthreads();
+        copyW(Wdh, Wdl);
+        __syncthreads();
 #pragma unroll
         for (int nt = 0; nt < 8; ++nt) {
-            const int base = (((nt << 2) | k0) << 9) + fb;
-            short8 bh = *(const short8*)&sWh[base];
-            short8 bl = *(const short8*)&sWl[base];
-            acc0[nt] = __builtin_amdgcn_mfma_f32_16x16x32_bf16(bh, ah0[k0], acc0[nt], 0, 0, 0);
-            acc0[nt] = __builtin_amdgcn_mfma_f32_16x16x32_bf16(bl, ah0[k0], acc0[nt], 0, 0, 0);
-            acc0[nt] = __builtin_amdgcn_mfma_f32_16x16x32_bf16(bh, al0[k0], acc0[nt], 0, 0, 0);
+            float4 bv = *(const float4*)(bm1 + nt * 16 + quad * 4);
+            acc0[nt][0] = bv.x; acc0[nt][1] = bv.y; acc0[nt][2] = bv.z; acc0[nt][3] = bv.w;
+            acc1[nt][0] = bv.x; acc1[nt][1] = bv.y; acc1[nt][2] = bv.z; acc1[nt][3] = bv.w;
+        }
+        mmacc(ph0, pl0, ph1, pl1);
+        {
+            float* d0 = Pd + (size_t)r0 * 128 + quad * 4;
+#pragma unroll
+            for (int nt = 0; nt < 8; ++nt)
+                *(float4*)(d0 + nt * 16) = make_float4(acc0[nt][0], acc0[nt][1], acc0[nt][2], acc0[nt][3]);
             if (h1) {
-                acc1[nt] = __builtin_amdgcn_mfma_f32_16x16x32_bf16(bh, ah1[k0], acc1[nt], 0, 0, 0);
-                acc1[nt] = __builtin_amdgcn_mfma_f32_16x16x32_bf16(bl, ah1[k0], acc1[nt], 0, 0, 0);
-                acc1[nt] = __builtin_amdgcn_mfma_f32_16x16x32_bf16(bh, al1[k0], acc1[nt], 0, 0, 0);
+                float* d1 = Pd + (size_t)r1 * 128 + quad * 4;
+#pragma unroll
+                for (int nt = 0; nt < 8; ++nt)
+                    *(float4*)(d1 + nt * 16) = make_float4(acc1[nt][0], acc1[nt][1], acc1[nt][2], acc1[nt][3]);
             }
         }
-    }
-    float p00 = 0.f, p01 = 0.f, p02 = 0.f, p10 = 0.f, p11 = 0.f, p12 = 0.f;
-#pragma unroll
-    for (int nt = 0; nt < 8; ++nt) {
-        float4 bv = *(const float4*)(bd1 + nt * 16 + quad * 4);
-#pragma unroll
-        for (int i = 0; i < 4; ++i) {
-            float b = (i == 0) ? bv.x : (i == 1) ? bv.y : (i == 2) ? bv.z : bv.w;
-            int c = nt * 16 + quad * 4 + i;
-            const float* wp = &Wd2[c * 3];
-            float v0 = fmaxf(acc0[nt][i] + b, 0.f);
-            float v1 = fmaxf(acc1[nt][i] + b, 0.f);
-            p00 += v0 * wp[0]; p01 += v0 * wp[1]; p02 += v0 * wp[2];
-            p10 += v1 * wp[0]; p11 += v1 * wp[1]; p12 += v1 * wp[2];
-        }
-    }
-    p00 += __shfl_xor(p00, 16); p00 += __shfl_xor(p00, 32);
-    p01 += __shfl_xor(p01, 16); p01 += __shfl_xor(p01, 32);
-    p02 += __shfl_xor(p02, 16); p02 += __shfl_xor(p02, 32);
-    p10 += __shfl_xor(p10, 16); p10 += __shfl_xor(p10, 32);
-    p11 += __shfl_xor(p11, 16); p11 += __shfl_xor(p11, 32);
-    p12 += __shfl_xor(p12, 16); p12 += __shfl_xor(p12, 32);
-    if (quad == 0) {
-        out[r0 * 3 + 0] = p00 + bd2[0];
-        out[r0 * 3 + 1] = p01 + bd2[1];
-        out[r0 * 3 + 2] = p02 + bd2[2];
-        if (h1) {
-            out[r1 * 3 + 0] = p10 + bd2[0];
-            out[r1 * 3 + 1] = p11 + bd2[1];
-            out[r1 * 3 + 2] = p12 + bd2[2];
+    } else {
+#pragma unroll
+        for (int k0 = 0; k0 < 4; ++k0) {
+            float v[8] = {acc0[2 * k0][0], acc0[2 * k0][1], acc0[2 * k0][2], acc0[2 * k0][3],
+                          acc0[2 * k0 + 1][0], acc0[2 * k0 + 1][1], acc0[2 * k0 + 1][2], acc0[2 * k0 + 1][3]};
+            cvt8(v, ph0[k0], pl0[k0]);
+        }
+#pragma unroll
+        for (int k0 = 0; k0 < 4; ++k0) {
+            float v[8] = {acc1[2 * k0][0], acc1[2 * k0][1], acc1[2 * k0][2], acc1[2 * k0][3],
+                          acc1[2 * k0 + 1][0], acc1[2 * k0 + 1][1], acc1[2 * k0 + 1][2], acc1[2 * k0 + 1][3]};
+            cvt8(v, ph1[k0], pl1[k0]);
+        }
+        __syncthreads();
+        copyW(Wdh, Wdl);
+        __syncthreads();
+#pragma unroll
+        for (int nt = 0; nt < 8; ++nt) {
+            float4 bv = *(const float4*)(bd1 + nt * 16 + quad * 4);
+            acc0[nt][0] = bv.x; acc0[nt][1] = bv.y; acc0[nt][2] = bv.z; acc0[nt][3] = bv.w;
+            acc1[nt][0] = bv.x; acc1[nt][1] = bv.y; acc1[nt][2] = bv.z; acc1[nt][3] = bv.w;
+        }
+        mmacc(ph0, pl0, ph1, pl1);
+        float p00 = 0.f, p01 = 0.f, p02 = 0.f, p10 = 0.f, p11 = 0.f, p12 = 0.f;
+#pragma unroll
+        for (int nt = 0; nt < 8; ++nt) {
+#pragma unroll
+            for (int i = 0; i < 4; ++i) {
+                int c = nt * 16 + quad * 4 + i;
+                const float* wp = &Wd2[c * 3];
+                float v0 = fmaxf(acc0[nt][i], 0.f);
+                float v1 = fmaxf(acc1[nt][i], 0.f);
+                p00 += v0 * wp[0]; p01 += v0 * wp[1]; p02 += v0 * wp[2];
+                p10 += v1 * wp[0]; p11 += v1 * wp[1]; p12 += v1 * wp[2];
+            }
+        }
+        p00 += __shfl_xor(p00, 16); p00 += __shfl_xor(p00, 32);
+        p01 += __shfl_xor(p01, 16); p01 += __shfl_xor(p01, 32);
+        p02 += __shfl_xor(p02, 16); p02 += __shfl_xor(p02, 32);
+        p10 += __shfl_xor(p10, 16); p10 += __shfl_xor(p10, 32);
+        p11 += __shfl_xor(p11, 16); p11 += __shfl_xor(p11, 32);
+        p12 += __shfl_xor(p12, 16); p12 += __shfl_xor(p12, 32);
+        if (quad == 0) {
+            outp[r0 * 3 + 0] = p00 + bd2[0];
+            outp[r0 * 3 + 1] = p01 + bd2[1];
+            outp[r0 * 3 + 2] = p02 + bd2[2];
+            if (h1) {
+                outp[r1 * 3 + 0] = p10 + bd2[0];
+                outp[r1 * 3 + 1] = p11 + bd2[1];
+                outp[r1 * 3 + 2] = p12 + bd2[2];
+            }
         }
     }
 }
@@ -985,7 +935,8 @@
     k_scatter<<<gE256, b256, 0, stream>>>(edge_index, edge_attr, cursor, src_sorted, ea_s);
     k_counts<<<NBLK, b256, 0, stream>>>(batch, x_mask, cnt_node, cnt_bc);
     k_genc<<<SGRID, b256, 0, stream>>>(x, x_mask, W_e1, b_e1, We2h, We2l, b_e2,
-                                       batch, h, part_h, part_hbc);
+                                       Wm1sh, Wm1sl, Wm1dh, Wm1dl, b_m1, batch,
+                                       h, Ps, Pd, part_h, part_hbc);
     k_redstats<<<GG, 128, 0, stream>>>(part_h, part_hbc, sum_h, sum_hbc);
 
     for (int rep = 0; rep < 3; ++rep) {
@@ -993,17 +944,18 @@
             k_gterm<false><<<GG, 128, 0, stream>>>(sum_h, sum_hbc, nullptr, cnt_node, cnt_bc, W_u1, gterm);
         else
             k_gterm<true><<<GG, 128, 0, stream>>>(nullptr, sum_hbc, partf, cnt_node, cnt_bc, W_u1, gterm);
-        k_gemm2<<<SGRID, b256, 0, stream>>>(h, Wm1sh, Wm1sl, Wm1dh, Wm1dl, b_m1, Ps, Pd);
         k_edge_agg<<<NN / 4, b256, 0, stream>>>(Ps, Pd, row_ptr, src_sorted, ea_s, W_m1, accm);
         if (rep < 2) {
-            k_fused3<true><<<SGRID, b256, 0, stream>>>(h, accm, Wu1ah, Wu1al, Wfh, Wfl,
-                                                       Wu2h, Wu2l, gterm, bfused, b_u2,
-                                                       batch, h, partf);
+            k_fused3<0><<<SGRID, b256, 0, stream>>>(h, accm, Wu1ah, Wu1al, Wfh, Wfl, Wu2h, Wu2l,
+                                                    Wm1sh, Wm1sl, Wm1dh, Wm1dl,
+                                                    gterm, bfused, b_u2, b_m1, nullptr, nullptr,
+                                                    nullptr, batch, h, Ps, Pd, partf, nullptr);
         } else {
-            k_fused3<false><<<SGRID, b256, 0, stream>>>(h, accm, Wu1ah, Wu1al, Wfh, Wfl,
-                                                        Wu2h, Wu2l, gterm, bfused, b_u2,
-                                                        batch, h, nullptr);
-        }
-    }
-    k_gdec<<<SGRID, b256, 0, stream>>>(h, Wd1h, Wd1l, b_d1, W_d2, b_d2, out);
-}
+            k_fused3<1><<<SGRID, b256, 0, stream>>>(h, accm, Wu1ah, Wu1al, Wfh, Wfl, Wu2h, Wu2l,
+                                                    nullptr, nullptr, Wd1h, Wd1l,
+                                                    gterm, bfused, b_u2, nullptr, b_d1, W_d2,
+                                                    b_d2, batch, nullptr, nullptr, nullptr,
+                                                    nullptr, out);
+        }
+    }
+}
```

Measured after the change: 626.6 us. -2.0%, faster.
